# Optimization experiments

Hardware: AMD Instinct MI355X
Metric: run time of the kernel (lower is better)

Reference implementation:

```python
import jax, jax.numpy as jnp
import numpy as np

D_MODEL = 768
N_HEADS = 12
CHUNK = 512
N_LM = 32
BATCH = 2
SEQ = 8192


def setup_inputs() -> dict:
    key = jax.random.key(0)
    ks = jax.random.split(key, 9)
    s = 1.0 / np.sqrt(D_MODEL)
    return {
        "x": jax.random.normal(ks[0], (BATCH, SEQ, D_MODEL), jnp.float32),
        "Wq": jax.random.normal(ks[1], (D_MODEL, D_MODEL), jnp.float32) * s,
        "bq": jax.random.normal(ks[2], (D_MODEL,), jnp.float32) * 0.01,
        "Wk": jax.random.normal(ks[3], (D_MODEL, D_MODEL), jnp.float32) * s,
        "bk": jax.random.normal(ks[4], (D_MODEL,), jnp.float32) * 0.01,
        "Wv": jax.random.normal(ks[5], (D_MODEL, D_MODEL), jnp.float32) * s,
        "bv": jax.random.normal(ks[6], (D_MODEL,), jnp.float32) * 0.01,
        "Wo": jax.random.normal(ks[7], (D_MODEL, D_MODEL), jnp.float32) * s,
        "bo": jax.random.normal(ks[8], (D_MODEL,), jnp.float32) * 0.01,
    }


def reference(x, Wq, bq, Wk, bk, Wv, bv, Wo, bo):
    B, S, D = x.shape
    H, hd = N_HEADS, D // N_HEADS
    scale = hd ** -0.5
    n_chunks = S // CHUNK  # SEQ chosen divisible by CHUNK -> no padding path

    # Global landmarks: mean-pool over N_LM evenly spaced segments
    seg = S // N_LM
    lm = x[:, : seg * N_LM, :].reshape(B, N_LM, seg, D).mean(axis=2)  # (B, L, D)

    # Q over local tokens only
    q = (x @ Wq.T + bq).reshape(B, n_chunks, CHUNK, H, hd)

    # K/V over [landmarks ++ local chunk]
    xc = x.reshape(B, n_chunks, CHUNK, D)
    lm_exp = jnp.broadcast_to(lm[:, None], (B, n_chunks, N_LM, D))
    kv = jnp.concatenate([lm_exp, xc], axis=2)  # (B, n_chunks, N_LM+CHUNK, D)
    k = (kv @ Wk.T + bk).reshape(B, n_chunks, N_LM + CHUNK, H, hd)
    v = (kv @ Wv.T + bv).reshape(B, n_chunks, N_LM + CHUNK, H, hd)

    attn = jnp.einsum("bnqhd,bnkhd->bnhqk", q, k) * scale
    attn = jax.nn.softmax(attn, axis=-1)  # dropout=0 (eval)
    out = jnp.einsum("bnhqk,bnkhd->bnqhd", attn, v).reshape(B, S, D)
    return out @ Wo.T + bo
```

## Files before the change

kernel.cpp:

```cpp
#include <hip/hip_runtime.h>
#include <cstdint>
#include <cstddef>

#define D_MODEL 768
#define N_HEADS 12
#define HEAD_DIM 64
#define CHUNK_SZ 512
#define N_LM 32
#define BATCH 2
#define SEQ 8192
#define N_CH 16
#define SEG 256
#define TOK (BATCH*SEQ)
#define MKV_PAD 16512
#define QSCALE 0.18033688011112042f

typedef unsigned short u16;
typedef __attribute__((ext_vector_type(8))) __bf16 bf16x8;
typedef __attribute__((ext_vector_type(4))) float f32x4;

__device__ __forceinline__ u16 f2bf(float f){
  unsigned u = __float_as_uint(f);
  u += 0x7fffu + ((u >> 16) & 1u);
  return (u16)(u >> 16);
}

__global__ __launch_bounds__(256) void cvt4_kernel(
    const float* __restrict__ w0, const float* __restrict__ w1,
    const float* __restrict__ w2, const float* __restrict__ w3,
    u16* __restrict__ o0, u16* __restrict__ o1, u16* __restrict__ o2, u16* __restrict__ o3)
{
  const int n4 = D_MODEL*D_MODEL/4;
  int i = blockIdx.x*256 + threadIdx.x;
  int sel = i / n4, j = i - sel*n4;
  const float* s = sel==0 ? w0 : sel==1 ? w1 : sel==2 ? w2 : w3;
  u16* o = sel==0 ? o0 : sel==1 ? o1 : sel==2 ? o2 : o3;
  float4 v = reinterpret_cast<const float4*>(s)[j];
  ushort4 p; p.x=f2bf(v.x); p.y=f2bf(v.y); p.z=f2bf(v.z); p.w=f2bf(v.w);
  reinterpret_cast<ushort4*>(o)[j] = p;
}

__global__ void build_xcat_kernel(const float* __restrict__ x, u16* __restrict__ xcat){
  const int total4 = MKV_PAD * D_MODEL / 4;
  const int x4 = TOK * D_MODEL / 4;
  int stride = gridDim.x * blockDim.x;
  for (int i = blockIdx.x*blockDim.x + threadIdx.x; i < total4; i += stride){
    ushort4 o;
    if (i < x4){
      float4 v = reinterpret_cast<const float4*>(x)[i];
      o.x = f2bf(v.x); o.y = f2bf(v.y); o.z = f2bf(v.z); o.w = f2bf(v.w);
    } else { o.x = 0; o.y = 0; o.z = 0; o.w = 0; }
    reinterpret_cast<ushort4*>(xcat)[i] = o;
  }
}

__global__ __launch_bounds__(256) void landmark_kernel(const float* __restrict__ x, u16* __restrict__ xcat){
  int b = blockIdx.x >> 5, l = blockIdx.x & 31;
  const float* base = x + ((size_t)b*SEQ + (size_t)l*SEG) * D_MODEL;
  int d = threadIdx.x;
  float a0=0.f, a1=0.f, a2=0.f;
  for (int tt=0; tt<SEG; ++tt){
    const float* row = base + (size_t)tt*D_MODEL;
    a0 += row[d]; a1 += row[d+256]; a2 += row[d+512];
  }
  u16* orow = xcat + ((size_t)TOK + (size_t)b*N_LM + l) * D_MODEL;
  const float inv = 1.f/(float)SEG;
  orow[d] = f2bf(a0*inv); orow[d+256] = f2bf(a1*inv); orow[d+512] = f2bf(a2*inv);
}

template<int OUT_F32, int BIAS_ROW>
__global__ __launch_bounds__(256) void gemm_bt_kernel(
    const u16* __restrict__ A, const u16* __restrict__ Bt,
    const float* __restrict__ bias, void* __restrict__ Cout, int ldc, float scale)
{
  __shared__ u16 As[128][72];
  __shared__ u16 Bs[128][72];
  const int t = threadIdx.x;
  const int lane = t & 63, wid = t >> 6;
  const int wr = wid >> 1, wc = wid & 1;
  const int lr = lane & 15, lg = lane >> 4;
  const size_t row0 = (size_t)blockIdx.x * 128;
  const int col0 = blockIdx.y * 128;

  f32x4 acc[4][4];
  #pragma unroll
  for (int m=0;m<4;m++)
    #pragma unroll
    for (int n=0;n<4;n++) acc[m][n] = f32x4{0.f,0.f,0.f,0.f};

  const int sc = (t & 7) << 3;
  const int sr0 = t >> 3;

  for (int ko = 0; ko < D_MODEL; ko += 64){
    #pragma unroll
    for (int i=0;i<4;i++){
      int r = sr0 + i*32;
      *reinterpret_cast<float4*>(&As[r][sc]) =
        *reinterpret_cast<const float4*>(&A[(row0 + r)*D_MODEL + ko + sc]);
      *reinterpret_cast<float4*>(&Bs[r][sc]) =
        *reinterpret_cast<const float4*>(&Bt[((size_t)col0 + r)*D_MODEL + ko + sc]);
    }
    __syncthreads();
    #pragma unroll
    for (int kk=0;kk<2;kk++){
      bf16x8 af[4], bv[4];
      #pragma unroll
      for (int m=0;m<4;m++)
        af[m] = *reinterpret_cast<const bf16x8*>(&As[wr*64 + m*16 + lr][kk*32 + lg*8]);
      #pragma unroll
      for (int n=0;n<4;n++)
        bv[n] = *reinterpret_cast<const bf16x8*>(&Bs[wc*64 + n*16 + lr][kk*32 + lg*8]);
      #pragma unroll
      for (int m=0;m<4;m++)
        #pragma unroll
        for (int n=0;n<4;n++)
          acc[m][n] = __builtin_amdgcn_mfma_f32_16x16x32_bf16(af[m], bv[n], acc[m][n], 0, 0, 0);
    }
    __syncthreads();
  }

  #pragma unroll
  for (int m=0;m<4;m++){
    #pragma unroll
    for (int n=0;n<4;n++){
      const int col = col0 + wc*64 + n*16 + lr;
      const float bcol = BIAS_ROW ? 0.f : bias[col];
      #pragma unroll
      for (int e=0;e<4;e++){
        size_t row = row0 + wr*64 + m*16 + lg*4 + e;
        float b = BIAS_ROW ? bias[row] : bcol;
        float val = (acc[m][n][e] + b) * scale;
        if (OUT_F32) reinterpret_cast<float*>(Cout)[row*(size_t)ldc + col] = val;
        else         reinterpret_cast<u16*>(Cout)[row*(size_t)ldc + col] = f2bf(val);
      }
    }
  }
}

template<int NK>
__device__ __forceinline__ void attn_compute(
    int lr, int lg,
    const u16 (* __restrict__ Ks)[72], const u16 (* __restrict__ Vs)[72],
    u16 (* __restrict__ Pw)[72],
    const bf16x8 (&qf)[2][2], float (&m_run)[2], float (&l_run)[2], f32x4 (&of)[2][4])
{
  constexpr int NCF = NK/16;
  constexpr int NKT = NK/32;

  f32x4 s2[2][NCF];
  #pragma unroll
  for (int c=0;c<NCF;c++){
    bf16x8 kf0 = *reinterpret_cast<const bf16x8*>(&Ks[c*16 + lr][lg*8]);
    bf16x8 kf1 = *reinterpret_cast<const bf16x8*>(&Ks[c*16 + lr][32 + lg*8]);
    #pragma unroll
    for (int r=0;r<2;r++){
      f32x4 s = f32x4{0.f,0.f,0.f,0.f};
      s = __builtin_amdgcn_mfma_f32_16x16x32_bf16(kf0, qf[r][0], s, 0,0,0);
      s = __builtin_amdgcn_mfma_f32_16x16x32_bf16(kf1, qf[r][1], s, 0,0,0);
      s2[r][c] = s;
    }
  }

  bf16x8 vf[NKT][4];
  #pragma unroll
  for (int kt=0;kt<NKT;kt++)
    #pragma unroll
    for (int c=0;c<4;c++)
      vf[kt][c] = *reinterpret_cast<const bf16x8*>(&Vs[c*16 + lr][kt*32 + lg*8]);

  #pragma unroll
  for (int r=0;r<2;r++){
    float tm = s2[r][0][0];
    #pragma unroll
    for (int c=0;c<NCF;c++)
      #pragma unroll
      for (int e=0;e<4;e++) tm = fmaxf(tm, s2[r][c][e]);
    tm = fmaxf(tm, __shfl_xor(tm, 16, 64));
    tm = fmaxf(tm, __shfl_xor(tm, 32, 64));
    float mnew = fmaxf(m_run[r], tm);
    float al = exp2f(m_run[r] - mnew);
    float ts = 0.f;
    #pragma unroll
    for (int c=0;c<NCF;c++)
      #pragma unroll
      for (int e=0;e<4;e++){
        float p = exp2f(s2[r][c][e] - mnew);
        s2[r][c][e] = p;
        ts += p;
      }
    ts += __shfl_xor(ts, 16, 64);
    ts += __shfl_xor(ts, 32, 64);
    l_run[r] = l_run[r]*al + ts;
    m_run[r] = mnew;
    #pragma unroll
    for (int c=0;c<4;c++)
      #pragma unroll
      for (int e=0;e<4;e++) of[r][c][e] *= al;

    #pragma unroll
    for (int c=0;c<NCF;c++){
      ushort4 pk;
      pk.x = f2bf(s2[r][c][0]); pk.y = f2bf(s2[r][c][1]);
      pk.z = f2bf(s2[r][c][2]); pk.w = f2bf(s2[r][c][3]);
      *reinterpret_cast<ushort4*>(&Pw[lr][c*16 + lg*4]) = pk;
    }
    #pragma unroll
    for (int kt=0;kt<NKT;kt++){
      bf16x8 pf = *reinterpret_cast<const bf16x8*>(&Pw[lr][kt*32 + lg*8]);
      #pragma unroll
      for (int c=0;c<4;c++)
        of[r][c] = __builtin_amdgcn_mfma_f32_16x16x32_bf16(vf[kt][c], pf, of[r][c], 0,0,0);
    }
  }
}

__global__ __launch_bounds__(256) void attn_kernel(
    const u16* __restrict__ Qb, const u16* __restrict__ Kb,
    const u16* __restrict__ Vt, u16* __restrict__ AO)
{
  __shared__ u16 Ks[64][72];
  __shared__ u16 Vs[64][72];
  __shared__ u16 PwAll[4][16][72];

  const int t = threadIdx.x;
  const int lane = t & 63, w = t >> 6;
  const int lr = lane & 15, lg = lane >> 4;
  const int qt = blockIdx.x;
  const int h  = blockIdx.y;
  const int b  = blockIdx.z >> 4, ch = blockIdx.z & 15;
  const size_t tok0 = (size_t)b*SEQ + (size_t)ch*CHUNK_SZ + (size_t)qt*128;
  const size_t bch0 = (size_t)b*SEQ + (size_t)ch*CHUNK_SZ;
  u16 (* __restrict__ Pw)[72] = PwAll[w];

  bf16x8 qf[2][2];
  #pragma unroll
  for (int r=0;r<2;r++)
    #pragma unroll
    for (int kk=0;kk<2;kk++)
      qf[r][kk] = *reinterpret_cast<const bf16x8*>(
          &Qb[(tok0 + w*32 + r*16 + lr)*D_MODEL + (size_t)h*HEAD_DIM + kk*32 + lg*8]);

  float m_run[2] = {-INFINITY, -INFINITY};
  float l_run[2] = {0.f, 0.f};
  f32x4 of[2][4];
  #pragma unroll
  for (int r=0;r<2;r++)
    #pragma unroll
    for (int c=0;c<4;c++) of[r][c] = f32x4{0.f,0.f,0.f,0.f};

  {
    const size_t lmrow0 = (size_t)TOK + (size_t)b*N_LM;
    int key = t >> 3, dc = (t & 7) << 3;
    *reinterpret_cast<bf16x8*>(&Ks[key][dc]) = *reinterpret_cast<const bf16x8*>(
        &Kb[(lmrow0 + key)*D_MODEL + (size_t)h*HEAD_DIM + dc]);
    int d = t >> 2, kc = (t & 3) << 3;
    *reinterpret_cast<bf16x8*>(&Vs[d][kc]) = *reinterpret_cast<const bf16x8*>(
        &Vt[((size_t)h*HEAD_DIM + d)*MKV_PAD + lmrow0 + kc]);
    __syncthreads();
    attn_compute<32>(lr, lg, Ks, Vs, Pw, qf, m_run, l_run, of);
  }

  bf16x8 kreg[2], vreg[2];
  const int key0 = t >> 3, dc0 = (t & 7) << 3;
  const int d0 = t >> 3, kc0 = (t & 7) << 3;
  {
    size_t col0 = bch0;
    kreg[0] = *reinterpret_cast<const bf16x8*>(&Kb[(col0 + key0)*D_MODEL + (size_t)h*HEAD_DIM + dc0]);
    kreg[1] = *reinterpret_cast<const bf16x8*>(&Kb[(col0 + key0 + 32)*D_MODEL + (size_t)h*HEAD_DIM + dc0]);
    vreg[0] = *reinterpret_cast<const bf16x8*>(&Vt[((size_t)h*HEAD_DIM + d0)*MKV_PAD + col0 + kc0]);
    vreg[1] = *reinterpret_cast<const bf16x8*>(&Vt[((size_t)h*HEAD_DIM + d0 + 32)*MKV_PAD + col0 + kc0]);
  }
  for (int tl = 0; tl < 8; ++tl){
    __syncthreads();
    *reinterpret_cast<bf16x8*>(&Ks[key0][dc0])      = kreg[0];
    *reinterpret_cast<bf16x8*>(&Ks[key0 + 32][dc0]) = kreg[1];
    *reinterpret_cast<bf16x8*>(&Vs[d0][kc0])        = vreg[0];
    *reinterpret_cast<bf16x8*>(&Vs[d0 + 32][kc0])   = vreg[1];
    __syncthreads();
    if (tl < 7){
      size_t col0 = bch0 + (size_t)(tl+1)*64;
      kreg[0] = *reinterpret_cast<const bf16x8*>(&Kb[(col0 + key0)*D_MODEL + (size_t)h*HEAD_DIM + dc0]);
      kreg[1] = *reinterpret_cast<const bf16x8*>(&Kb[(col0 + key0 + 32)*D_MODEL + (size_t)h*HEAD_DIM + dc0]);
      vreg[0] = *reinterpret_cast<const bf16x8*>(&Vt[((size_t)h*HEAD_DIM + d0)*MKV_PAD + col0 + kc0]);
      vreg[1] = *reinterpret_cast<const bf16x8*>(&Vt[((size_t)h*HEAD_DIM + d0 + 32)*MKV_PAD + col0 + kc0]);
    }
    attn_compute<64>(lr, lg, Ks, Vs, Pw, qf, m_run, l_run, of);
  }

  #pragma unroll
  for (int r=0;r<2;r++){
    float inv = 1.f / l_run[r];
    size_t row = (tok0 + w*32 + r*16 + lr)*D_MODEL + (size_t)h*HEAD_DIM;
    #pragma unroll
    for (int c=0;c<4;c++){
      ushort4 pk;
      pk.x = f2bf(of[r][c][0]*inv); pk.y = f2bf(of[r][c][1]*inv);
      pk.z = f2bf(of[r][c][2]*inv); pk.w = f2bf(of[r][c][3]*inv);
      *reinterpret_cast<ushort4*>(&AO[row + c*16 + lg*4]) = pk;
    }
  }
}

extern "C" void kernel_launch(void* const* d_in, const int* in_sizes, int n_in,
                              void* d_out, int out_size, void* d_ws, size_t ws_size,
                              hipStream_t stream) {
  const float* x  = (const float*)d_in[0];
  const float* Wq = (const float*)d_in[1];
  const float* bq = (const float*)d_in[2];
  const float* Wk = (const float*)d_in[3];
  const float* bk = (const float*)d_in[4];
  const float* Wv = (const float*)d_in[5];
  const float* bv = (const float*)d_in[6];
  const float* Wo = (const float*)d_in[7];
  const float* bo = (const float*)d_in[8];
  float* out = (float*)d_out;

  const size_t XCAT_OFF = 0;
  const size_t Q_OFF    = 25362432;
  const size_t K_OFF    = 50528256;
  const size_t VT_OFF   = 75890688;
  const size_t AO_OFF   = 101253120;
  const size_t WQ_OFF   = 126418944;
  const size_t WK_OFF   = 127598592;
  const size_t WV_OFF   = 128778240;
  const size_t WO_OFF   = 129957888;
  const size_t TOTAL    = 131137536;
  if (ws_size < TOTAL) return;

  char* ws = (char*)d_ws;
  u16* xcat = (u16*)(ws + XCAT_OFF);
  u16* Qb   = (u16*)(ws + Q_OFF);
  u16* Kb   = (u16*)(ws + K_OFF);
  u16* Vt   = (u16*)(ws + VT_OFF);
  u16* AO   = (u16*)(ws + AO_OFF);
  u16* wqb  = (u16*)(ws + WQ_OFF);
  u16* wkb  = (u16*)(ws + WK_OFF);
  u16* wvb  = (u16*)(ws + WV_OFF);
  u16* wob  = (u16*)(ws + WO_OFF);

  dim3 blk(256);
  cvt4_kernel<<<dim3(2304), blk, 0, stream>>>(Wq, Wk, Wv, Wo, wqb, wkb, wvb, wob);
  build_xcat_kernel<<<dim3(4096), blk, 0, stream>>>(x, xcat);
  landmark_kernel<<<dim3(64), blk, 0, stream>>>(x, xcat);

  gemm_bt_kernel<0,0><<<dim3(128, 6), blk, 0, stream>>>(xcat, wqb, bq, (void*)Qb, D_MODEL, QSCALE);
  gemm_bt_kernel<0,0><<<dim3(129, 6), blk, 0, stream>>>(xcat, wkb, bk, (void*)Kb, D_MODEL, 1.f);
  gemm_bt_kernel<0,1><<<dim3(6, 129), blk, 0, stream>>>(wvb, xcat, bv, (void*)Vt, MKV_PAD, 1.f);

  attn_kernel<<<dim3(4, 12, 32), blk, 0, stream>>>(Qb, Kb, Vt, AO);

  gemm_bt_kernel<1,0><<<dim3(128, 6), blk, 0, stream>>>(AO, wob, bo, (void*)out, D_MODEL, 1.f);
}
```

Baseline: 250.5 us.

## Fuse Q/K projections, split landmark reduction, defer softmax rescale, use native bf16 cvt

Q and K projections now run in one GEMM launch over a concatenated weight buffer (Wq and Wk converted contiguously), with the epilogue picking the destination and scale. The landmark mean is split into a 512-block partial-sum kernel and a small final kernel, so it no longer runs on only 64 blocks. Online softmax skips rescaling the running max and accumulators unless the new max exceeds the old by a threshold, cutting exp and multiply work. Float-to-bf16 conversion switches to the compiler's native cast. Risks: overflow headroom assumptions in the deferred rescale, and reusing the AO buffer as scratch for landmark partials.

```diff
diff --git a/kernel.cpp b/kernel.cpp
--- a/kernel.cpp
+++ b/kernel.cpp
@@ -14,15 +14,14 @@
 #define TOK (BATCH*SEQ)
 #define MKV_PAD 16512
 #define QSCALE 0.18033688011112042f
+#define DEFER_THR 12.0f
 
 typedef unsigned short u16;
 typedef __attribute__((ext_vector_type(8))) __bf16 bf16x8;
 typedef __attribute__((ext_vector_type(4))) float f32x4;
 
-__device__ __forceinline__ u16 f2bf(float f){
-  unsigned u = __float_as_uint(f);
-  u += 0x7fffu + ((u >> 16) & 1u);
-  return (u16)(u >> 16);
+__device__ __forceinline__ u16 f2bf_rn(float f){
+  union { __bf16 b; u16 u; } c; c.b = (__bf16)f; return c.u;
 }
 
 __global__ __launch_bounds__(256) void cvt4_kernel(
@@ -36,7 +35,7 @@
   const float* s = sel==0 ? w0 : sel==1 ? w1 : sel==2 ? w2 : w3;
   u16* o = sel==0 ? o0 : sel==1 ? o1 : sel==2 ? o2 : o3;
   float4 v = reinterpret_cast<const float4*>(s)[j];
-  ushort4 p; p.x=f2bf(v.x); p.y=f2bf(v.y); p.z=f2bf(v.z); p.w=f2bf(v.w);
+  ushort4 p; p.x=f2bf_rn(v.x); p.y=f2bf_rn(v.y); p.z=f2bf_rn(v.z); p.w=f2bf_rn(v.w);
   reinterpret_cast<ushort4*>(o)[j] = p;
 }
 
@@ -48,24 +47,37 @@
     ushort4 o;
     if (i < x4){
       float4 v = reinterpret_cast<const float4*>(x)[i];
-      o.x = f2bf(v.x); o.y = f2bf(v.y); o.z = f2bf(v.z); o.w = f2bf(v.w);
+      o.x = f2bf_rn(v.x); o.y = f2bf_rn(v.y); o.z = f2bf_rn(v.z); o.w = f2bf_rn(v.w);
     } else { o.x = 0; o.y = 0; o.z = 0; o.w = 0; }
     reinterpret_cast<ushort4*>(xcat)[i] = o;
   }
 }
 
-__global__ __launch_bounds__(256) void landmark_kernel(const float* __restrict__ x, u16* __restrict__ xcat){
-  int b = blockIdx.x >> 5, l = blockIdx.x & 31;
-  const float* base = x + ((size_t)b*SEQ + (size_t)l*SEG) * D_MODEL;
+__global__ __launch_bounds__(256) void lm_part_kernel(const float* __restrict__ x, float* __restrict__ lmp){
+  int seg = blockIdx.x >> 3, sub = blockIdx.x & 7;
+  int b = seg >> 5, l = seg & 31;
+  const float* base = x + ((size_t)b*SEQ + (size_t)l*SEG + (size_t)sub*32) * D_MODEL;
   int d = threadIdx.x;
   float a0=0.f, a1=0.f, a2=0.f;
-  for (int tt=0; tt<SEG; ++tt){
+  for (int tt=0; tt<32; ++tt){
     const float* row = base + (size_t)tt*D_MODEL;
     a0 += row[d]; a1 += row[d+256]; a2 += row[d+512];
   }
-  u16* orow = xcat + ((size_t)TOK + (size_t)b*N_LM + l) * D_MODEL;
+  float* orow = lmp + (size_t)blockIdx.x * D_MODEL;
+  orow[d] = a0; orow[d+256] = a1; orow[d+512] = a2;
+}
+__global__ __launch_bounds__(256) void lm_final_kernel(const float* __restrict__ lmp, u16* __restrict__ xcat){
+  int seg = blockIdx.x;
+  int d = threadIdx.x;
+  float a0=0.f, a1=0.f, a2=0.f;
+  #pragma unroll
+  for (int i=0;i<8;i++){
+    const float* p = lmp + ((size_t)seg*8 + i)*D_MODEL;
+    a0 += p[d]; a1 += p[d+256]; a2 += p[d+512];
+  }
+  u16* orow = xcat + ((size_t)TOK + seg)*D_MODEL;
   const float inv = 1.f/(float)SEG;
-  orow[d] = f2bf(a0*inv); orow[d+256] = f2bf(a1*inv); orow[d+512] = f2bf(a2*inv);
+  orow[d] = f2bf_rn(a0*inv); orow[d+256] = f2bf_rn(a1*inv); orow[d+512] = f2bf_rn(a2*inv);
 }
 
 template<int OUT_F32, int BIAS_ROW>
@@ -131,7 +143,80 @@
         float b = BIAS_ROW ? bias[row] : bcol;
         float val = (acc[m][n][e] + b) * scale;
         if (OUT_F32) reinterpret_cast<float*>(Cout)[row*(size_t)ldc + col] = val;
-        else         reinterpret_cast<u16*>(Cout)[row*(size_t)ldc + col] = f2bf(val);
+        else         reinterpret_cast<u16*>(Cout)[row*(size_t)ldc + col] = f2bf_rn(val);
+      }
+    }
+  }
+}
+
+__global__ __launch_bounds__(256) void gemm_qk_kernel(
+    const u16* __restrict__ A, const u16* __restrict__ Wqk,
+    const float* __restrict__ bq, const float* __restrict__ bk,
+    u16* __restrict__ Qb, u16* __restrict__ Kb)
+{
+  __shared__ u16 As[128][72];
+  __shared__ u16 Bs[128][72];
+  const int t = threadIdx.x;
+  const int lane = t & 63, wid = t >> 6;
+  const int wr = wid >> 1, wc = wid & 1;
+  const int lr = lane & 15, lg = lane >> 4;
+  const size_t row0 = (size_t)blockIdx.x * 128;
+  const int col0 = blockIdx.y * 128;
+  const bool isk = col0 >= 768;
+
+  f32x4 acc[4][4];
+  #pragma unroll
+  for (int m=0;m<4;m++)
+    #pragma unroll
+    for (int n=0;n<4;n++) acc[m][n] = f32x4{0.f,0.f,0.f,0.f};
+
+  const int sc = (t & 7) << 3;
+  const int sr0 = t >> 3;
+
+  for (int ko = 0; ko < D_MODEL; ko += 64){
+    #pragma unroll
+    for (int i=0;i<4;i++){
+      int r = sr0 + i*32;
+      *reinterpret_cast<float4*>(&As[r][sc]) =
+        *reinterpret_cast<const float4*>(&A[(row0 + r)*D_MODEL + ko + sc]);
+      *reinterpret_cast<float4*>(&Bs[r][sc]) =
+        *reinterpret_cast<const float4*>(&Wqk[((size_t)col0 + r)*D_MODEL + ko + sc]);
+    }
+    __syncthreads();
+    #pragma unroll
+    for (int kk=0;kk<2;kk++){
+      bf16x8 af[4], bv[4];
+      #pragma unroll
+      for (int m=0;m<4;m++)
+        af[m] = *reinterpret_cast<const bf16x8*>(&As[wr*64 + m*16 + lr][kk*32 + lg*8]);
+      #pragma unroll
+      for (int n=0;n<4;n++)
+        bv[n] = *reinterpret_cast<const bf16x8*>(&Bs[wc*64 + n*16 + lr][kk*32 + lg*8]);
+      #pragma unroll
+      for (int m=0;m<4;m++)
+        #pragma unroll
+        for (int n=0;n<4;n++)
+          acc[m][n] = __builtin_amdgcn_mfma_f32_16x16x32_bf16(af[m], bv[n], acc[m][n], 0, 0, 0);
+    }
+    __syncthreads();
+  }
+
+  const float scale = isk ? 1.f : QSCALE;
+  u16* dst = isk ? Kb : Qb;
+  #pragma unroll
+  for (int m=0;m<4;m++){
+    #pragma unroll
+    for (int n=0;n<4;n++){
+      const int col = col0 + wc*64 + n*16 + lr;
+      const int ocol = isk ? col - 768 : col;
+      const float b = isk ? bk[ocol] : bq[ocol];
+      #pragma unroll
+      for (int e=0;e<4;e++){
+        size_t row = row0 + wr*64 + m*16 + lg*4 + e;
+        if (isk || row < TOK){
+          float val = (acc[m][n][e] + b) * scale;
+          dst[row*D_MODEL + ocol] = f2bf_rn(val);
+        }
       }
     }
   }
@@ -177,31 +262,34 @@
       for (int e=0;e<4;e++) tm = fmaxf(tm, s2[r][c][e]);
     tm = fmaxf(tm, __shfl_xor(tm, 16, 64));
     tm = fmaxf(tm, __shfl_xor(tm, 32, 64));
-    float mnew = fmaxf(m_run[r], tm);
-    float al = exp2f(m_run[r] - mnew);
+    if (!__all(tm - m_run[r] <= DEFER_THR)){
+      float mnew = fmaxf(m_run[r], tm);
+      float al = exp2f(m_run[r] - mnew);
+      m_run[r] = mnew;
+      l_run[r] *= al;
+      #pragma unroll
+      for (int c=0;c<4;c++)
+        #pragma unroll
+        for (int e=0;e<4;e++) of[r][c][e] *= al;
+    }
     float ts = 0.f;
     #pragma unroll
     for (int c=0;c<NCF;c++)
       #pragma unroll
       for (int e=0;e<4;e++){
-        float p = exp2f(s2[r][c][e] - mnew);
+        float p = exp2f(s2[r][c][e] - m_run[r]);
         s2[r][c][e] = p;
         ts += p;
       }
     ts += __shfl_xor(ts, 16, 64);
     ts += __shfl_xor(ts, 32, 64);
-    l_run[r] = l_run[r]*al + ts;
-    m_run[r] = mnew;
-    #pragma unroll
-    for (int c=0;c<4;c++)
-      #pragma unroll
-      for (int e=0;e<4;e++) of[r][c][e] *= al;
+    l_run[r] += ts;
 
     #pragma unroll
     for (int c=0;c<NCF;c++){
       ushort4 pk;
-      pk.x = f2bf(s2[r][c][0]); pk.y = f2bf(s2[r][c][1]);
-      pk.z = f2bf(s2[r][c][2]); pk.w = f2bf(s2[r][c][3]);
+      pk.x = f2bf_rn(s2[r][c][0]); pk.y = f2bf_rn(s2[r][c][1]);
+      pk.z = f2bf_rn(s2[r][c][2]); pk.w = f2bf_rn(s2[r][c][3]);
       *reinterpret_cast<ushort4*>(&Pw[lr][c*16 + lg*4]) = pk;
     }
     #pragma unroll
@@ -294,8 +382,8 @@
     #pragma unroll
     for (int c=0;c<4;c++){
       ushort4 pk;
-      pk.x = f2bf(of[r][c][0]*inv); pk.y = f2bf(of[r][c][1]*inv);
-      pk.z = f2bf(of[r][c][2]*inv); pk.w = f2bf(of[r][c][3]*inv);
+      pk.x = f2bf_rn(of[r][c][0]*inv); pk.y = f2bf_rn(of[r][c][1]*inv);
+      pk.z = f2bf_rn(of[r][c][2]*inv); pk.w = f2bf_rn(of[r][c][3]*inv);
       *reinterpret_cast<ushort4*>(&AO[row + c*16 + lg*4]) = pk;
     }
   }
@@ -333,18 +421,19 @@
   u16* Kb   = (u16*)(ws + K_OFF);
   u16* Vt   = (u16*)(ws + VT_OFF);
   u16* AO   = (u16*)(ws + AO_OFF);
-  u16* wqb  = (u16*)(ws + WQ_OFF);
+  float* lmp = (float*)(ws + AO_OFF);
+  u16* wqkb = (u16*)(ws + WQ_OFF);
   u16* wkb  = (u16*)(ws + WK_OFF);
   u16* wvb  = (u16*)(ws + WV_OFF);
   u16* wob  = (u16*)(ws + WO_OFF);
 
   dim3 blk(256);
-  cvt4_kernel<<<dim3(2304), blk, 0, stream>>>(Wq, Wk, Wv, Wo, wqb, wkb, wvb, wob);
+  cvt4_kernel<<<dim3(2304), blk, 0, stream>>>(Wq, Wk, Wv, Wo, wqkb, wkb, wvb, wob);
   build_xcat_kernel<<<dim3(4096), blk, 0, stream>>>(x, xcat);
-  landmark_kernel<<<dim3(64), blk, 0, stream>>>(x, xcat);
-
-  gemm_bt_kernel<0,0><<<dim3(128, 6), blk, 0, stream>>>(xcat, wqb, bq, (void*)Qb, D_MODEL, QSCALE);
-  gemm_bt_kernel<0,0><<<dim3(129, 6), blk, 0, stream>>>(xcat, wkb, bk, (void*)Kb, D_MODEL, 1.f);
+  lm_part_kernel<<<dim3(512), blk, 0, stream>>>(x, lmp);
+  lm_final_kernel<<<dim3(64), blk, 0, stream>>>(lmp, xcat);
+
+  gemm_qk_kernel<<<dim3(129, 12), blk, 0, stream>>>(xcat, wqkb, bq, bk, Qb, Kb);
   gemm_bt_kernel<0,1><<<dim3(6, 129), blk, 0, stream>>>(wvb, xcat, bv, (void*)Vt, MKV_PAD, 1.f);
 
   attn_kernel<<<dim3(4, 12, 32), blk, 0, stream>>>(Qb, Kb, Vt, AO);
```

New measurement: 254.0 us. No clear change (+1.4%).
